# Performance work log

Hardware: AMD Instinct MI355X
Metric: run time of the kernel (lower is better)

## Reference

```python
import jax, jax.numpy as jnp
import numpy as np

NUM_HEADS = 32

def setup_inputs() -> dict:
    key = jax.random.key(0)
    ks = jax.random.split(key, 5)
    B, S, D = 2, 2048, 1024
    d = D // NUM_HEADS  # 32
    return {
        "x": jax.random.normal(ks[0], (B, S, D), dtype=jnp.float32),
        "wq": jax.random.normal(ks[1], (d, d), dtype=jnp.float32) / np.sqrt(d),
        "bq": jnp.zeros((d,), dtype=jnp.float32),
        "wk": jax.random.normal(ks[2], (d, d), dtype=jnp.float32) / np.sqrt(d),
        "bk": jnp.zeros((d,), dtype=jnp.float32),
        "wv": jax.random.normal(ks[3], (d, d), dtype=jnp.float32) / np.sqrt(d),
        "bv": jnp.zeros((d,), dtype=jnp.float32),
        "wo": jax.random.normal(ks[4], (D, D), dtype=jnp.float32) / np.sqrt(D),
        "bo": jnp.zeros((D,), dtype=jnp.float32),
    }

def reference(x, wq, bq, wk, bk, wv, bv, wo, bo):
    B, S, D = x.shape
    H = NUM_HEADS
    d = D // H
    # split heads: [B, S, H, d] -> [B, H, S, d]
    h = x.reshape(B, S, H, d).transpose(0, 2, 1, 3)
    # shared per-head Q/K/V projections (single SelfAttention submodule)
    q = jnp.einsum('bhsd,de->bhse', h, wq) + bq
    k = jnp.einsum('bhsd,de->bhse', h, wk) + bk
    v = jnp.einsum('bhsd,de->bhse', h, wv) + bv
    scale = 1.0 / jnp.sqrt(jnp.asarray(d, dtype=x.dtype))
    scores = jnp.einsum('bhqd,bhkd->bhqk', q, k) * scale  # [B,H,S,S]
    attn = jax.nn.softmax(scores, axis=-1)
    out = jnp.einsum('bhqk,bhkd->bhqd', attn, v)  # [B,H,S,d]
    # concat heads -> [B, S, D]
    concat = out.transpose(0, 2, 1, 3).reshape(B, S, D)
    return concat @ wo + bo
```

## Files before the change

kernel.cpp:

```cpp
#include <hip/hip_runtime.h>
#include <hip/hip_bf16.h>

typedef __attribute__((ext_vector_type(8))) short bf16x8;
typedef __attribute__((ext_vector_type(4))) short bf16x4;
typedef __attribute__((ext_vector_type(4))) float f32x4;

#if defined(__has_builtin)
#if __has_builtin(__builtin_amdgcn_exp2f)
#define EXP2F(x) __builtin_amdgcn_exp2f(x)
#else
#define EXP2F(x) exp2f(x)
#endif
#else
#define EXP2F(x) exp2f(x)
#endif

#define S_LEN 2048
#define NH 32
#define HD 32
#define DMODEL 1024
#define NB 2

static __device__ __forceinline__ unsigned int cvt_pk_bf16(float lo, float hi) {
    unsigned int r;
    asm("v_cvt_pk_bf16_f32 %0, %1, %2" : "=v"(r) : "v"(lo), "v"(hi));
    return r;
}

__global__ __launch_bounds__(256) void qkv_stage(
    const float* __restrict__ x,
    const float* __restrict__ wq, const float* __restrict__ bq,
    const float* __restrict__ wk, const float* __restrict__ bk,
    const float* __restrict__ wv, const float* __restrict__ bv,
    __hip_bfloat16* __restrict__ qws,
    __hip_bfloat16* __restrict__ kws,
    __hip_bfloat16* __restrict__ vtws)
{
    const int tid = threadIdx.x;
    const int cg  = blockIdx.y;
    const int rb  = blockIdx.x;
    const int c   = cg * 256 + tid;
    const int h   = c >> 5;
    const int e   = c & 31;
    const int row0 = rb * 16;
    const int b   = row0 >> 11;
    const int s0  = row0 & 2047;

    float wqc[32], wkc[32], wvc[32];
#pragma unroll
    for (int d = 0; d < 32; ++d) {
        wqc[d] = wq[d * 32 + e];
        wkc[d] = wk[d * 32 + e];
        wvc[d] = wv[d * 32 + e];
    }
    const float bqv = bq[e], bkv = bk[e], bvv = bv[e];

    __shared__ float xl[16][256];
#pragma unroll
    for (int r = 0; r < 16; ++r)
        xl[r][tid] = x[((size_t)b * S_LEN + s0 + r) * DMODEL + cg * 256 + tid];
    __syncthreads();

    const float SC = 0.1767766953f * 1.44269504089f;
    const int hl = (tid >> 5) * 32;

    float vreg[16];
#pragma unroll
    for (int r = 0; r < 16; ++r) {
        float aq = bqv, ak = bkv, av = bvv;
#pragma unroll
        for (int d = 0; d < 32; ++d) {
            float xv = xl[r][hl + d];
            aq += xv * wqc[d];
            ak += xv * wkc[d];
            av += xv * wvc[d];
        }
        size_t base = ((size_t)(b * NH + h) * S_LEN + (s0 + r)) * HD + e;
        qws[base] = __float2bfloat16(aq * SC);
        kws[base] = __float2bfloat16(ak);
        vreg[r] = av;
    }

    unsigned int pk[8];
#pragma unroll
    for (int i = 0; i < 8; ++i) {
        __hip_bfloat16 t0 = __float2bfloat16(vreg[2 * i]);
        __hip_bfloat16 t1 = __float2bfloat16(vreg[2 * i + 1]);
        unsigned short u0 = *reinterpret_cast<unsigned short*>(&t0);
        unsigned short u1 = *reinterpret_cast<unsigned short*>(&t1);
        pk[i] = (unsigned int)u0 | ((unsigned int)u1 << 16);
    }
    size_t vbase = ((size_t)(b * NH + h) * HD + e) * S_LEN + s0;
    *reinterpret_cast<uint4*>(vtws + vbase)     = make_uint4(pk[0], pk[1], pk[2], pk[3]);
    *reinterpret_cast<uint4*>(vtws + vbase + 8) = make_uint4(pk[4], pk[5], pk[6], pk[7]);
}

__global__ __launch_bounds__(256) void wo_transpose(
    const float* __restrict__ wo, __hip_bfloat16* __restrict__ wot)
{
    __shared__ float t[64][65];
    const int bx = blockIdx.x;
    const int by = blockIdx.y;
    const int tid = threadIdx.x;
    const int col = tid & 63, row4 = tid >> 6;
#pragma unroll
    for (int i = 0; i < 16; ++i) {
        int r = i * 4 + row4;
        t[r][col] = wo[(size_t)(bx * 64 + r) * DMODEL + by * 64 + col];
    }
    __syncthreads();
#pragma unroll
    for (int i = 0; i < 16; ++i) {
        int r = i * 4 + row4;
        wot[(size_t)(by * 64 + r) * DMODEL + bx * 64 + col] =
            __float2bfloat16(t[col][r]);
    }
}

__global__ __launch_bounds__(256) void attn_kernel(
    const __hip_bfloat16* __restrict__ qws,
    const __hip_bfloat16* __restrict__ kws,
    const __hip_bfloat16* __restrict__ vtws,
    __hip_bfloat16* __restrict__ cws)
{
    const int tid = threadIdx.x;
    const int w  = tid >> 6;
    const int ln = tid & 63;
    const int lg = ln >> 4;
    const int lm = ln & 15;

    const int bi  = blockIdx.x;
    const int xcd = bi & 7;
    const int idx = bi >> 3;
    const int qt  = idx & 31;
    const int bh  = (xcd << 3) | (idx >> 5);
    const int b   = bh >> 5;
    const int h   = bh & 31;

    const __hip_bfloat16* qp = qws + (size_t)bh * S_LEN * HD;
    const char* kpb = (const char*)(kws  + (size_t)bh * S_LEN * HD);
    const char* vpb = (const char*)(vtws + (size_t)bh * HD * S_LEN);

    const int qr0 = qt * 64 + w * 16;

    bf16x8 qb = *reinterpret_cast<const bf16x8*>(qp + (size_t)(qr0 + lm) * HD + lg * 8);

    __shared__ __align__(16) char kv[8192];
    __shared__ __align__(16) __hip_bfloat16 plds_all[4][16][72];
    __hip_bfloat16 (*plds)[72] = plds_all[w];

    f32x4 l4 = {0.f, 0.f, 0.f, 0.f};
    f32x4 o0 = {0.f, 0.f, 0.f, 0.f};
    f32x4 o1 = {0.f, 0.f, 0.f, 0.f};
    const f32x4 zoff = {-8.f, -8.f, -8.f, -8.f};

    const int vrow  = tid >> 3;
    const int vslot = tid & 7;
    const size_t vsrc = (size_t)vrow * (S_LEN * 2) +
                        (size_t)(vslot ^ (vrow & 7)) * 16;

    uint4 kreg = *reinterpret_cast<const uint4*>(kpb + tid * 16);
    uint4 vreg = *reinterpret_cast<const uint4*>(vpb + vsrc);

    for (int kt = 0; kt < S_LEN / 64; ++kt) {
        if (kt) __syncthreads();
        *reinterpret_cast<uint4*>(&kv[tid * 16])        = kreg;
        *reinterpret_cast<uint4*>(&kv[4096 + tid * 16]) = vreg;
        __syncthreads();
        if (kt + 1 < S_LEN / 64) {
            kreg = *reinterpret_cast<const uint4*>(
                kpb + (size_t)(kt + 1) * 4096 + tid * 16);
            vreg = *reinterpret_cast<const uint4*>(
                vpb + vsrc + (size_t)(kt + 1) * 128);
        }

        f32x4 s[4];
#pragma unroll
        for (int c = 0; c < 4; ++c) {
            bf16x8 kf = *reinterpret_cast<const bf16x8*>(
                &kv[c * 1024 + lm * 64 + lg * 16]);
            s[c] = __builtin_amdgcn_mfma_f32_16x16x32_bf16(kf, qb, zoff, 0, 0, 0);
        }

#pragma unroll
        for (int c = 0; c < 4; ++c) {
            float p0 = EXP2F(s[c][0]);
            float p1 = EXP2F(s[c][1]);
            float p2 = EXP2F(s[c][2]);
            float p3 = EXP2F(s[c][3]);
            l4[0] += p0; l4[1] += p1; l4[2] += p2; l4[3] += p3;
            *reinterpret_cast<uint2*>(&plds[lm][c * 16 + lg * 4]) =
                make_uint2(cvt_pk_bf16(p0, p1), cvt_pk_bf16(p2, p3));
        }

#pragma unroll
        for (int ks = 0; ks < 2; ++ks) {
            bf16x8 pa = *reinterpret_cast<const bf16x8*>(
                &plds[lm][ks * 32 + lg * 8]);
            int j = (ks * 4 + lg) ^ (lm & 7);
            bf16x8 va = *reinterpret_cast<const bf16x8*>(
                &kv[4096 + lm * 128 + j * 16]);
            o0 = __builtin_amdgcn_mfma_f32_16x16x32_bf16(va, pa, o0, 0, 0, 0);
            bf16x8 vb = *reinterpret_cast<const bf16x8*>(
                &kv[4096 + (lm + 16) * 128 + j * 16]);
            o1 = __builtin_amdgcn_mfma_f32_16x16x32_bf16(vb, pa, o1, 0, 0, 0);
        }
    }

    float l = (l4[0] + l4[1]) + (l4[2] + l4[3]);
    l += __shfl_xor(l, 16);
    l += __shfl_xor(l, 32);
    float inv = 1.0f / l;

    __hip_bfloat16* cb = cws + ((size_t)b * S_LEN + qr0 + lm) * DMODEL + h * HD;
    union { unsigned int u[2]; bf16x4 v; } w0, w1;
    w0.u[0] = cvt_pk_bf16(o0[0] * inv, o0[1] * inv);
    w0.u[1] = cvt_pk_bf16(o0[2] * inv, o0[3] * inv);
    w1.u[0] = cvt_pk_bf16(o1[0] * inv, o1[1] * inv);
    w1.u[1] = cvt_pk_bf16(o1[2] * inv, o1[3] * inv);
    *reinterpret_cast<bf16x4*>(cb + lg * 4)      = w0.v;
    *reinterpret_cast<bf16x4*>(cb + 16 + lg * 4) = w1.v;
}

__global__ __launch_bounds__(256) void out_gemm(
    const __hip_bfloat16* __restrict__ A,
    const __hip_bfloat16* __restrict__ Bt,
    const float* __restrict__ bo,
    float* __restrict__ out)
{
    const int tid = threadIdx.x;
    const int ln = tid & 63;
    const int w  = tid >> 6;
    const int lg = ln >> 4, lm = ln & 15;
    const int wr = w >> 1, wc = w & 1;
    const int bi = blockIdx.x;
    const int bn = bi & 7;
    const int bm = bi >> 3;
    const int r0 = bm * 64;
    const int n0 = bn * 128;

    __shared__ __align__(16) char lds[24576];

    f32x4 acc[2][4];
#pragma unroll
    for (int m = 0; m < 2; ++m)
#pragma unroll
        for (int n = 0; n < 4; ++n)
            acc[m][n] = {0.f, 0.f, 0.f, 0.f};

    const int srow = tid >> 3;
    const int sj   = tid & 7;
    const int swo  = srow * 128 + ((sj ^ (srow & 7)) << 4);

    const __hip_bfloat16* Ab = A  + (size_t)r0 * DMODEL;
    const __hip_bfloat16* Bb = Bt + (size_t)n0 * DMODEL;

    uint4 ar0 = *reinterpret_cast<const uint4*>(Ab + (size_t)srow        * DMODEL + sj * 8);
    uint4 ar1 = *reinterpret_cast<const uint4*>(Ab + (size_t)(srow + 32) * DMODEL + sj * 8);
    uint4 br0 = *reinterpret_cast<const uint4*>(Bb + (size_t)srow        * DMODEL + sj * 8);
    uint4 br1 = *reinterpret_cast<const uint4*>(Bb + (size_t)(srow + 32) * DMODEL + sj * 8);
    uint4 br2 = *reinterpret_cast<const uint4*>(Bb + (size_t)(srow + 64) * DMODEL + sj * 8);
    uint4 br3 = *reinterpret_cast<const uint4*>(Bb + (size_t)(srow + 96) * DMODEL + sj * 8);

    for (int k0 = 0; k0 < DMODEL; k0 += 64) {
        if (k0) __syncthreads();
        *reinterpret_cast<uint4*>(&lds[swo])          = ar0;
        *reinterpret_cast<uint4*>(&lds[swo + 4096])   = ar1;
        *reinterpret_cast<uint4*>(&lds[8192 + swo])           = br0;
        *reinterpret_cast<uint4*>(&lds[8192 + swo + 4096])    = br1;
        *reinterpret_cast<uint4*>(&lds[8192 + swo + 8192])    = br2;
        *reinterpret_cast<uint4*>(&lds[8192 + swo + 12288])   = br3;
        __syncthreads();
        if (k0 + 64 < DMODEL) {
            const __hip_bfloat16* An = Ab + k0 + 64;
            const __hip_bfloat16* Bn = Bb + k0 + 64;
            ar0 = *reinterpret_cast<const uint4*>(An + (size_t)srow        * DMODEL + sj * 8);
            ar1 = *reinterpret_cast<const uint4*>(An + (size_t)(srow + 32) * DMODEL + sj * 8);
            br0 = *reinterpret_cast<const uint4*>(Bn + (size_t)srow        * DMODEL + sj * 8);
            br1 = *reinterpret_cast<const uint4*>(Bn + (size_t)(srow + 32) * DMODEL + sj * 8);
            br2 = *reinterpret_cast<const uint4*>(Bn + (size_t)(srow + 64) * DMODEL + sj * 8);
            br3 = *reinterpret_cast<const uint4*>(Bn + (size_t)(srow + 96) * DMODEL + sj * 8);
        }

#pragma unroll
        for (int kh = 0; kh < 2; ++kh) {
            bf16x8 af[2], bf[4];
#pragma unroll
            for (int m = 0; m < 2; ++m) {
                int row = wr * 32 + m * 16 + lm;
                af[m] = *reinterpret_cast<const bf16x8*>(
                    &lds[row * 128 + (((kh * 4 + lg) ^ (row & 7)) << 4)]);
            }
#pragma unroll
            for (int n = 0; n < 4; ++n) {
                int row = wc * 64 + n * 16 + lm;
                bf[n] = *reinterpret_cast<const bf16x8*>(
                    &lds[8192 + row * 128 + (((kh * 4 + lg) ^ (row & 7)) << 4)]);
            }
#pragma unroll
            for (int m = 0; m < 2; ++m)
#pragma unroll
                for (int n = 0; n < 4; ++n)
                    acc[m][n] = __builtin_amdgcn_mfma_f32_16x16x32_bf16(
                        af[m], bf[n], acc[m][n], 0, 0, 0);
        }
    }

#pragma unroll
    for (int n = 0; n < 4; ++n) {
        int col = n0 + wc * 64 + n * 16 + lm;
        float bv = bo[col];
#pragma unroll
        for (int m = 0; m < 2; ++m) {
#pragma unroll
            for (int r = 0; r < 4; ++r) {
                int row = r0 + wr * 32 + m * 16 + lg * 4 + r;
                out[(size_t)row * DMODEL + col] = acc[m][n][r] + bv;
            }
        }
    }
}

extern "C" void kernel_launch(void* const* d_in, const int* in_sizes, int n_in,
                              void* d_out, int out_size, void* d_ws, size_t ws_size,
                              hipStream_t stream)
{
    const float* x  = (const float*)d_in[0];
    const float* wq = (const float*)d_in[1];
    const float* bq = (const float*)d_in[2];
    const float* wk = (const float*)d_in[3];
    const float* bk = (const float*)d_in[4];
    const float* wv = (const float*)d_in[5];
    const float* bv = (const float*)d_in[6];
    const float* wo = (const float*)d_in[7];
    const float* bo = (const float*)d_in[8];
    float* out = (float*)d_out;

    char* ws = (char*)d_ws;
    __hip_bfloat16* qws  = (__hip_bfloat16*)(ws);
    __hip_bfloat16* kws  = (__hip_bfloat16*)(ws + ((size_t)8  << 20));
    __hip_bfloat16* vtws = (__hip_bfloat16*)(ws + ((size_t)16 << 20));
    __hip_bfloat16* cws  = (__hip_bfloat16*)(ws + ((size_t)24 << 20));
    __hip_bfloat16* wot  = (__hip_bfloat16*)(ws + ((size_t)32 << 20));

    qkv_stage<<<dim3(NB * S_LEN / 16, 4), 256, 0, stream>>>(
        x, wq, bq, wk, bk, wv, bv, qws, kws, vtws);
    wo_transpose<<<dim3(16, 16), 256, 0, stream>>>(wo, wot);
    attn_kernel<<<NB * NH * (S_LEN / 64), 256, 0, stream>>>(qws, kws, vtws, cws);
    out_gemm<<<(NB * S_LEN / 64) * (DMODEL / 128), 256, 0, stream>>>(
        cws, wot, bo, out);
}
```

Baseline: 116.7 us.

## Compute per-head QKV projection with bf16 MFMA instead of scalar FMAs

Rewrites the QKV projection stage to use 16x16x32 bf16 MFMA instructions. Each wave handles two heads for a 16-token tile. x is converted to bf16 in registers and multiplied against the bf16 Wq/Wk/Wv fragments, with the softmax scale folded into Wq and bq. V is computed as Wv^T·x^T so the transposed V layout falls out directly. This removes the scalar FMA loop and the shared-memory staging of x. In exchange, x and the weights are rounded to bf16 before the projection, and stores become scattered 2-byte writes.

```diff
diff --git a/kernel.cpp b/kernel.cpp
--- a/kernel.cpp
+++ b/kernel.cpp
@@ -27,7 +27,7 @@
     return r;
 }
 
-__global__ __launch_bounds__(256) void qkv_stage(
+__global__ __launch_bounds__(256) void qkv_mfma(
     const float* __restrict__ x,
     const float* __restrict__ wq, const float* __restrict__ bq,
     const float* __restrict__ wk, const float* __restrict__ bk,
@@ -37,62 +37,75 @@
     __hip_bfloat16* __restrict__ vtws)
 {
     const int tid = threadIdx.x;
-    const int cg  = blockIdx.y;
-    const int rb  = blockIdx.x;
-    const int c   = cg * 256 + tid;
-    const int h   = c >> 5;
-    const int e   = c & 31;
-    const int row0 = rb * 16;
-    const int b   = row0 >> 11;
-    const int s0  = row0 & 2047;
-
-    float wqc[32], wkc[32], wvc[32];
-#pragma unroll
-    for (int d = 0; d < 32; ++d) {
-        wqc[d] = wq[d * 32 + e];
-        wkc[d] = wk[d * 32 + e];
-        wvc[d] = wv[d * 32 + e];
-    }
-    const float bqv = bq[e], bkv = bk[e], bvv = bv[e];
-
-    __shared__ float xl[16][256];
-#pragma unroll
-    for (int r = 0; r < 16; ++r)
-        xl[r][tid] = x[((size_t)b * S_LEN + s0 + r) * DMODEL + cg * 256 + tid];
-    __syncthreads();
+    const int w  = tid >> 6;
+    const int ln = tid & 63;
+    const int lg = ln >> 4, lm = ln & 15;
+
+    const int bi = blockIdx.x;
+    const int tb = bi >> 2;
+    const int hq = bi & 3;
+    const int t0 = tb * 16;
+    const int b  = t0 >> 11;
+    const int s0 = t0 & 2047;
 
     const float SC = 0.1767766953f * 1.44269504089f;
-    const int hl = (tid >> 5) * 32;
-
-    float vreg[16];
-#pragma unroll
-    for (int r = 0; r < 16; ++r) {
-        float aq = bqv, ak = bkv, av = bvv;
-#pragma unroll
-        for (int d = 0; d < 32; ++d) {
-            float xv = xl[r][hl + d];
-            aq += xv * wqc[d];
-            ak += xv * wkc[d];
-            av += xv * wvc[d];
-        }
-        size_t base = ((size_t)(b * NH + h) * S_LEN + (s0 + r)) * HD + e;
-        qws[base] = __float2bfloat16(aq * SC);
-        kws[base] = __float2bfloat16(ak);
-        vreg[r] = av;
-    }
-
-    unsigned int pk[8];
-#pragma unroll
-    for (int i = 0; i < 8; ++i) {
-        __hip_bfloat16 t0 = __float2bfloat16(vreg[2 * i]);
-        __hip_bfloat16 t1 = __float2bfloat16(vreg[2 * i + 1]);
-        unsigned short u0 = *reinterpret_cast<unsigned short*>(&t0);
-        unsigned short u1 = *reinterpret_cast<unsigned short*>(&t1);
-        pk[i] = (unsigned int)u0 | ((unsigned int)u1 << 16);
-    }
-    size_t vbase = ((size_t)(b * NH + h) * HD + e) * S_LEN + s0;
-    *reinterpret_cast<uint4*>(vtws + vbase)     = make_uint4(pk[0], pk[1], pk[2], pk[3]);
-    *reinterpret_cast<uint4*>(vtws + vbase + 8) = make_uint4(pk[4], pk[5], pk[6], pk[7]);
+
+    bf16x8 wqB[2], wkB[2], wvA[2];
+    f32x4 bqC[2], bkC[2], bvC[2];
+#pragma unroll
+    for (int et = 0; et < 2; ++et) {
+        const int e = et * 16 + lm;
+        union { unsigned int u4[4]; bf16x8 v; } tq, tk, tv;
+#pragma unroll
+        for (int jj = 0; jj < 4; ++jj) {
+            int k0 = lg * 8 + jj * 2;
+            tq.u4[jj] = cvt_pk_bf16(wq[k0 * 32 + e] * SC, wq[(k0 + 1) * 32 + e] * SC);
+            tk.u4[jj] = cvt_pk_bf16(wk[k0 * 32 + e],      wk[(k0 + 1) * 32 + e]);
+            tv.u4[jj] = cvt_pk_bf16(wv[k0 * 32 + e],      wv[(k0 + 1) * 32 + e]);
+        }
+        wqB[et] = tq.v; wkB[et] = tk.v; wvA[et] = tv.v;
+
+        float bqe = bq[e] * SC;
+        float bke = bk[e];
+        bqC[et] = (f32x4){bqe, bqe, bqe, bqe};
+        bkC[et] = (f32x4){bke, bke, bke, bke};
+#pragma unroll
+        for (int r = 0; r < 4; ++r)
+            bvC[et][r] = bv[et * 16 + lg * 4 + r];
+    }
+
+#pragma unroll
+    for (int u = 0; u < 2; ++u) {
+        const int h = hq * 8 + w * 2 + u;
+
+        const float* xp = x + (size_t)(t0 + lm) * DMODEL + h * 32 + lg * 8;
+        float4 xlo = *reinterpret_cast<const float4*>(xp);
+        float4 xhi = *reinterpret_cast<const float4*>(xp + 4);
+        union { unsigned int u4[4]; bf16x8 v; } xa;
+        xa.u4[0] = cvt_pk_bf16(xlo.x, xlo.y);
+        xa.u4[1] = cvt_pk_bf16(xlo.z, xlo.w);
+        xa.u4[2] = cvt_pk_bf16(xhi.x, xhi.y);
+        xa.u4[3] = cvt_pk_bf16(xhi.z, xhi.w);
+
+        const int bh = b * NH + h;
+        __hip_bfloat16* qrow = qws + ((size_t)bh * S_LEN + s0) * HD;
+        __hip_bfloat16* krow = kws + ((size_t)bh * S_LEN + s0) * HD;
+        __hip_bfloat16* vrow = vtws + (size_t)bh * HD * S_LEN + s0;
+
+#pragma unroll
+        for (int et = 0; et < 2; ++et) {
+            f32x4 qd = __builtin_amdgcn_mfma_f32_16x16x32_bf16(xa.v, wqB[et], bqC[et], 0, 0, 0);
+            f32x4 kd = __builtin_amdgcn_mfma_f32_16x16x32_bf16(xa.v, wkB[et], bkC[et], 0, 0, 0);
+            f32x4 vd = __builtin_amdgcn_mfma_f32_16x16x32_bf16(wvA[et], xa.v, bvC[et], 0, 0, 0);
+#pragma unroll
+            for (int r = 0; r < 4; ++r) {
+                int srow = 4 * lg + r;
+                qrow[(size_t)srow * HD + et * 16 + lm] = __float2bfloat16(qd[r]);
+                krow[(size_t)srow * HD + et * 16 + lm] = __float2bfloat16(kd[r]);
+                vrow[(size_t)(et * 16 + 4 * lg + r) * S_LEN + lm] = __float2bfloat16(vd[r]);
+            }
+        }
+    }
 }
 
 __global__ __launch_bounds__(256) void wo_transpose(
@@ -343,7 +356,7 @@
     __hip_bfloat16* cws  = (__hip_bfloat16*)(ws + ((size_t)24 << 20));
     __hip_bfloat16* wot  = (__hip_bfloat16*)(ws + ((size_t)32 << 20));
 
-    qkv_stage<<<dim3(NB * S_LEN / 16, 4), 256, 0, stream>>>(
+    qkv_mfma<<<1024, 256, 0, stream>>>(
         x, wq, bq, wk, bk, wv, bv, qws, kws, vtws);
     wo_transpose<<<dim3(16, 16), 256, 0, stream>>>(wo, wot);
     attn_kernel<<<NB * NH * (S_LEN / 64), 256, 0, stream>>>(qws, kws, vtws, cws);
```

Measured after the change: 97.49 us. -16.4%, faster.
